# Optimization experiments

Measured on AMD Instinct MI355X. Metric: run time of the kernel, lower is better.

## Reference

```python
import jax, jax.numpy as jnp
import numpy as np

N, R, E, H, D_MAX = 1024, 8192, 1024, 4, 48
DH = E // H
P_EDGE = 16.0 / R  # average in-degree ~16


def setup_inputs() -> dict:
    key = jax.random.key(0)
    ks = jax.random.split(key, 6)
    s = 0.02
    return {
        "target": jax.random.normal(ks[0], (N, E), jnp.float32),
        "source": jax.random.normal(ks[1], (R, E), jnp.float32),
        "adj": (jax.random.uniform(ks[2], (N, R)) < P_EDGE).astype(jnp.float32),
        "W_trans": jax.random.normal(ks[3], (E, E), jnp.float32) * s,
        "b_trans": jnp.zeros((E,), jnp.float32),
        "in_proj_w": jax.random.normal(ks[4], (3 * E, E), jnp.float32) * s,
        "in_proj_b": jnp.zeros((3 * E,), jnp.float32),
        "out_w": jax.random.normal(ks[5], (E, E), jnp.float32) * s,
        "out_b": jnp.zeros((E,), jnp.float32),
        "unit_id": 0,
    }


def reference(target, source, adj, W_trans, b_trans, in_proj_w, in_proj_b, out_w, out_b, unit_id):
    # source = relu(trans_fc(source))
    src = jax.nn.relu(source @ W_trans.T + b_trans)  # [R, E]

    # build padded neighbor index lists (torch loops per node; here vectorized)
    deg = adj.sum(axis=1).astype(jnp.int32)                # [N]
    order = jnp.argsort(-adj, axis=1)[:, :D_MAX]           # stable: 1-columns first, ascending col idx
    valid = jnp.arange(D_MAX)[None, :] < deg[:, None]      # [N, D] True = real neighbor
    neigh = jnp.where(valid, order, 0)                     # pad with index 0 (masked, like torch)
    kv_in = src[neigh]                                     # [N, D, E] gathered neighbor feats

    # nn.MultiheadAttention: q=target (len-1 query), k=v=padded neighbors
    Wq, Wk, Wv = jnp.split(in_proj_w, 3, axis=0)
    bq, bk, bv = jnp.split(in_proj_b, 3)
    q = (target @ Wq.T + bq).reshape(-1, H, DH)            # [N, H, dh]
    k = (kv_in @ Wk.T + bk).reshape(-1, D_MAX, H, DH)      # [N, D, H, dh]
    v = (kv_in @ Wv.T + bv).reshape(-1, D_MAX, H, DH)

    scores = jnp.einsum('nhd,nkhd->nhk', q, k) / np.float32(np.sqrt(DH))  # [N, H, D]
    # key_padding_mask: padded slots -> -inf; give zero-degree nodes one dummy
    # unmasked slot so softmax stays finite (their output is zeroed below)
    safe_valid = valid.at[:, 0].set(valid[:, 0] | (deg == 0))
    scores = jnp.where(safe_valid[:, None, :], scores, -jnp.inf)
    attn = jax.nn.softmax(scores, axis=-1)
    out = jnp.einsum('nhk,nkhd->nhd', attn, v).reshape(-1, E)
    out = out @ out_w.T + out_b

    # scatter back: inactive (degree-0) nodes stay zero, like att_res_padded
    return jnp.where((deg > 0)[:, None], out, jnp.zeros((), out.dtype))
```

## Files before the change

### kernel.cpp

```cpp
#include <hip/hip_runtime.h>

#define N_NODES 1024
#define R_SRC   8192
#define E_DIM   1024
#define H_HEADS 4
#define DH_DIM  256
#define D_MAXN  48

typedef __attribute__((ext_vector_type(8))) short short8;
typedef __attribute__((ext_vector_type(4))) float f32x4;

__device__ __forceinline__ unsigned short f2bf(float f) {
    unsigned u = __float_as_uint(f);
    unsigned r = u + 0x7fffu + ((u >> 16) & 1u);
    return (unsigned short)(r >> 16);
}
__device__ __forceinline__ float bf2f(unsigned short b) {
    return __uint_as_float(((unsigned)b) << 16);
}
__device__ __forceinline__ void gload16(const void* g, void* l) {
    __builtin_amdgcn_global_load_lds(
        (const __attribute__((address_space(1))) unsigned int*)g,
        (__attribute__((address_space(3))) unsigned int*)l,
        16, 0, 0);
}
template<int N> __device__ __forceinline__ void vwait() {
    if constexpr (N == 8)       asm volatile("s_waitcnt vmcnt(8)" ::: "memory");
    else if constexpr (N == 6)  asm volatile("s_waitcnt vmcnt(6)" ::: "memory");
    else if constexpr (N == 1)  asm volatile("s_waitcnt vmcnt(1)" ::: "memory");
    else                        asm volatile("s_waitcnt vmcnt(0)" ::: "memory");
}

struct GD {
    const unsigned short* A;
    const unsigned short* B;
    const float* bias;
    void* C;
    int N, K, nbx, relu, outbf;
    const int* rowmask;
};

template<int BM, int BN>
__global__ __launch_bounds__(512) void gemm_t(GD d0, GD d1, int split)
{
    constexpr int AI = BM / 64;
    constexpr int BI = BN / 64;
    constexpr int VN = AI + BI;
    constexpr int FM = BM / 32;
    constexpr int FN = BN / 64;

    __shared__ __align__(16) unsigned short lds[3][(BM + BN) * 64];

    int bid = blockIdx.x;
    const int nwg = gridDim.x;
    bid = (bid & 7) * (nwg >> 3) + (bid >> 3);

    GD d; int q;
    if (bid < split) { d = d0; q = bid; }
    else             { d = d1; q = bid - split; }
    const int m0 = (q / d.nbx) * BM;
    const int n0 = (q % d.nbx) * BN;
    const int K  = d.K;

    const int t = threadIdx.x;
    const int w = t >> 6, l = t & 63;
    const int wm = w >> 2, wn = w & 3;

    const int trow = t >> 3, tkc = t & 7;
    const int tswz = tkc ^ (trow & 7);
    const unsigned short* gA[AI];
    const unsigned short* gB[BI];
#pragma unroll
    for (int i = 0; i < AI; ++i)
        gA[i] = d.A + (size_t)(m0 + i * 64 + trow) * K + tswz * 8;
#pragma unroll
    for (int i = 0; i < BI; ++i)
        gB[i] = d.B + (size_t)(n0 + i * 64 + trow) * K + tswz * 8;

    f32x4 acc[FM][FN] = {};

    auto STAGE = [&](int c, int kt) {
        const int ko = kt * 64;
#pragma unroll
        for (int i = 0; i < AI; ++i)
            gload16(gA[i] + ko, &lds[c][(i * 512 + t) * 8]);
#pragma unroll
        for (int i = 0; i < BI; ++i)
            gload16(gB[i] + ko, &lds[c][BM * 64 + (i * 512 + t) * 8]);
    };

    const int nt = K / 64;
    STAGE(0, 0);
    STAGE(1, 1);
    vwait<VN>();
    __builtin_amdgcn_s_barrier();

    const int lr = l & 15, hi = l >> 4;
    const int rsw = l & 7;
    const int cs0 = ((0 + hi) ^ rsw) * 8;
    const int cs1 = ((4 + hi) ^ rsw) * 8;
    const int abase = (wm * (BM / 2) + lr) * 64;
    const int bbase = BM * 64 + (wn * 64 + lr) * 64;

    for (int kt = 0; kt < nt; ++kt) {
        const int cur = kt % 3;
        if (kt + 2 < nt) STAGE((kt + 2) % 3, kt + 2);

        const unsigned short* Ls = &lds[cur][0];

        short8 bv[FN][2];
#pragma unroll
        for (int fj = 0; fj < FN; ++fj) {
            bv[fj][0] = *(const short8*)&Ls[bbase + fj * 1024 + cs0];
            bv[fj][1] = *(const short8*)&Ls[bbase + fj * 1024 + cs1];
        }
#pragma unroll
        for (int g = 0; g < FM; g += 4) {
            short8 av[4][2];
#pragma unroll
            for (int fi = 0; fi < 4; ++fi) {
                av[fi][0] = *(const short8*)&Ls[abase + (g + fi) * 1024 + cs0];
                av[fi][1] = *(const short8*)&Ls[abase + (g + fi) * 1024 + cs1];
            }
            __builtin_amdgcn_s_setprio(1);
#pragma unroll
            for (int ks = 0; ks < 2; ++ks)
#pragma unroll
                for (int fi = 0; fi < 4; ++fi)
#pragma unroll
                    for (int fj = 0; fj < FN; ++fj)
                        acc[g + fi][fj] = __builtin_amdgcn_mfma_f32_16x16x32_bf16(
                            av[fi][ks], bv[fj][ks], acc[g + fi][fj], 0, 0, 0);
            __builtin_amdgcn_s_setprio(0);
        }

        asm volatile("" ::: "memory");
        __builtin_amdgcn_s_barrier();
        if (kt + 2 < nt) {
            vwait<VN>();
        } else {
            vwait<0>();
        }
        __builtin_amdgcn_s_barrier();
    }

#pragma unroll
    for (int fj = 0; fj < FN; ++fj) {
        const int c = n0 + wn * 64 + fj * 16 + lr;
        const float bvs = d.bias[c];
#pragma unroll
        for (int fi = 0; fi < FM; ++fi) {
            const int rb = m0 + wm * (BM / 2) + fi * 16 + hi * 4;
#pragma unroll
            for (int qq = 0; qq < 4; ++qq) {
                const int r = rb + qq;
                float x = acc[fi][fj][qq] + bvs;
                if (d.relu) x = fmaxf(x, 0.0f);
                if (d.rowmask && d.rowmask[r] == 0) x = 0.0f;
                if (d.outbf) ((unsigned short*)d.C)[(size_t)r * d.N + c] = f2bf(x);
                else         ((float*)d.C)[(size_t)r * d.N + c] = x;
            }
        }
    }
}

struct GS {
    const unsigned short* A;
    const unsigned short* B;
    const float* bias;
    void* C;
    int lda, ldb, ldc, K, relu, outbf;
    long long azs, bzs, czs;
    int bias_zs;
    const int* rowmask;
};

__global__ __launch_bounds__(256) void gemm_s(GS g)
{
    const int z = blockIdx.z;
    const unsigned short* A = g.A + (size_t)((long long)z * g.azs);
    const unsigned short* B = g.B + (size_t)((long long)z * g.bzs);
    const float* bias = g.bias ? g.bias + (size_t)z * g.bias_zs : nullptr;

    __shared__ __align__(16) unsigned short S[128 * 32];

    const int t = threadIdx.x;
    const int m0 = blockIdx.y * 64;
    const int n0 = blockIdx.x * 64;
    const int w = t >> 6, l = t & 63;
    const int wrow = (w >> 1) * 32;
    const int wcol = (w & 1) * 32;
    const int lr = l & 15;
    const int kg = (l >> 4) * 8;

    f32x4 acc[2][2] = {};

    const unsigned short* gp[2];
    unsigned short* lp[2];
    {
        const int c0 = t;
        gp[0] = A + (size_t)(m0 + (c0 >> 2)) * g.lda + (c0 & 3) * 8;
        lp[0] = &S[c0 * 8];
        const int c1 = t;
        gp[1] = B + (size_t)(n0 + (c1 >> 2)) * g.ldb + (c1 & 3) * 8;
        lp[1] = &S[2048 + c1 * 8];
    }

    for (int k0 = 0; k0 < g.K; k0 += 32) {
        gload16(gp[0] + k0, lp[0]);
        gload16(gp[1] + k0, lp[1]);
        __syncthreads();

        short8 af[2], bw[2];
#pragma unroll
        for (int i = 0; i < 2; ++i)
            af[i] = *(const short8*)&S[(wrow + i * 16 + lr) * 32 + kg];
#pragma unroll
        for (int j = 0; j < 2; ++j)
            bw[j] = *(const short8*)&S[2048 + (wcol + j * 16 + lr) * 32 + kg];
#pragma unroll
        for (int i = 0; i < 2; ++i)
#pragma unroll
            for (int j = 0; j < 2; ++j)
                acc[i][j] = __builtin_amdgcn_mfma_f32_16x16x32_bf16(
                    af[i], bw[j], acc[i][j], 0, 0, 0);
        __syncthreads();
    }

#pragma unroll
    for (int j = 0; j < 2; ++j) {
        const int c = n0 + wcol + j * 16 + lr;
        const float bv = bias ? bias[c] : 0.0f;
#pragma unroll
        for (int i = 0; i < 2; ++i) {
            const int rbase = m0 + wrow + i * 16 + (l >> 4) * 4;
#pragma unroll
            for (int qq = 0; qq < 4; ++qq) {
                const int r = rbase + qq;
                float x = acc[i][j][qq] + bv;
                if (g.relu) x = fmaxf(x, 0.0f);
                if (g.rowmask && g.rowmask[r] == 0) x = 0.0f;
                if (g.outbf)
                    ((unsigned short*)g.C)[(size_t)((long long)z * g.czs) + (size_t)r * g.ldc + c] = f2bf(x);
                else
                    ((float*)g.C)[(size_t)((long long)z * g.czs) + (size_t)r * g.ldc + c] = x;
            }
        }
    }
}

struct ConvArgs {
    const float* s[6];
    unsigned short* d[6];
    unsigned off[7];
};

__global__ __launch_bounds__(256) void pre_kernel(
    const float* __restrict__ adj, int* __restrict__ neigh, int* __restrict__ deg,
    ConvArgs a, const float* __restrict__ inw_f, unsigned short* __restrict__ WkT,
    int nconv)
{
    const int t = threadIdx.x;

    if (blockIdx.x >= (unsigned)(N_NODES + nconv)) {
        __shared__ float tile[64][65];
        const int tb = blockIdx.x - N_NODES - nconv;
        const int h = tb >> 6, rem = tb & 63;
        const int e0 = (rem >> 2) * 64, d0 = (rem & 3) * 64;
        const int r = t >> 2, c4 = (t & 3) * 16;
        const float* tsrc = inw_f + (size_t)(E_DIM + h * 256 + d0 + r) * E_DIM + e0 + c4;
#pragma unroll
        for (int jj = 0; jj < 4; ++jj) {
            float4 v = ((const float4*)tsrc)[jj];
            tile[r][c4 + jj * 4 + 0] = v.x;
            tile[r][c4 + jj * 4 + 1] = v.y;
            tile[r][c4 + jj * 4 + 2] = v.z;
            tile[r][c4 + jj * 4 + 3] = v.w;
        }
        __syncthreads();
        const int er = t >> 2, dc = (t & 3) * 16;
        unsigned short* wout = WkT + ((size_t)h * E_DIM + e0 + er) * 256 + d0 + dc;
#pragma unroll
        for (int jj = 0; jj < 4; ++jj) {
            ushort4 o;
            o.x = f2bf(tile[dc + jj * 4 + 0][er]);
            o.y = f2bf(tile[dc + jj * 4 + 1][er]);
            o.z = f2bf(tile[dc + jj * 4 + 2][er]);
            o.w = f2bf(tile[dc + jj * 4 + 3][er]);
            ((ushort4*)wout)[jj] = o;
        }
        return;
    }

    if (blockIdx.x >= (unsigned)N_NODES) {
        unsigned i = (blockIdx.x - N_NODES) * 256 + t;
        if (i >= a.off[6]) return;
        int seg = 0;
#pragma unroll
        for (int s = 1; s < 6; ++s) seg += (i >= a.off[s]);
        unsigned j = i - a.off[seg];
        float4 v = ((const float4*)a.s[seg])[j];
        ushort4 o;
        o.x = f2bf(v.x); o.y = f2bf(v.y); o.z = f2bf(v.z); o.w = f2bf(v.w);
        ((ushort4*)a.d[seg])[j] = o;
        return;
    }

    const int n    = blockIdx.x;
    const int w    = t >> 6;
    const int lane = t & 63;
    const float* row = adj + (size_t)n * R_SRC;

    __shared__ int s_cnt[4];
    __shared__ int s_idx[4][D_MAXN];

    const int seg0 = w * (R_SRC / 4);
    const unsigned long long lower = (1ULL << lane) - 1ULL;
    int total = 0;

    for (int base = seg0; base < seg0 + R_SRC / 4; base += 256) {
        const float v0 = row[base + lane];
        const float v1 = row[base + 64 + lane];
        const float v2 = row[base + 128 + lane];
        const float v3 = row[base + 192 + lane];
        const unsigned long long m0 = __ballot(v0 != 0.0f);
        const unsigned long long m1 = __ballot(v1 != 0.0f);
        const unsigned long long m2 = __ballot(v2 != 0.0f);
        const unsigned long long m3 = __ballot(v3 != 0.0f);
        int p;
        p = total + __popcll(m0 & lower);
        if (v0 != 0.0f && p < D_MAXN) s_idx[w][p] = base + lane;
        total += __popcll(m0);
        p = total + __popcll(m1 & lower);
        if (v1 != 0.0f && p < D_MAXN) s_idx[w][p] = base + 64 + lane;
        total += __popcll(m1);
        p = total + __popcll(m2 & lower);
        if (v2 != 0.0f && p < D_MAXN) s_idx[w][p] = base + 128 + lane;
        total += __popcll(m2);
        p = total + __popcll(m3 & lower);
        if (v3 != 0.0f && p < D_MAXN) s_idx[w][p] = base + 192 + lane;
        total += __popcll(m3);
    }
    if (lane == 0) s_cnt[w] = total;
    __syncthreads();

    int start = 0;
#pragma unroll
    for (int i = 0; i < 4; ++i) if (i < w) start += s_cnt[i];
    const int degree = s_cnt[0] + s_cnt[1] + s_cnt[2] + s_cnt[3];
    const int nstore = total < D_MAXN ? total : D_MAXN;
    if (lane < nstore) {
        const int gpos = start + lane;
        if (gpos < D_MAXN) neigh[n * D_MAXN + gpos] = s_idx[w][lane];
    }
    if (t == 0) deg[n] = degree;
}

__global__ __launch_bounds__(256) void gather_ctx(
    const float* __restrict__ Ahat, const unsigned short* __restrict__ srcrel,
    const int* __restrict__ neigh, const int* __restrict__ deg,
    unsigned short* __restrict__ ctx)
{
    const int n = blockIdx.x;
    const int t = threadIdx.x;
    const int h = t >> 6;
    const int lane = t & 63;

    unsigned short* crow = ctx + ((size_t)n * H_HEADS + h) * E_DIM + lane * 16;
    const int degree = deg[n];
    if (degree == 0) {
        ushort4 z4 = {0, 0, 0, 0};
#pragma unroll
        for (int j = 0; j < 4; ++j) ((ushort4*)crow)[j] = z4;
        return;
    }
    const int dv = degree < D_MAXN ? degree : D_MAXN;

    __shared__ int s_neigh[D_MAXN];
    if (t < dv) s_neigh[t] = neigh[n * D_MAXN + t];
    __syncthreads();

    float a[16];
    {
        const float4* ap = (const float4*)(Ahat + (size_t)n * (H_HEADS * E_DIM) + h * E_DIM + lane * 16);
#pragma unroll
        for (int j = 0; j < 4; ++j) {
            float4 v = ap[j];
            a[j * 4 + 0] = v.x; a[j * 4 + 1] = v.y; a[j * 4 + 2] = v.z; a[j * 4 + 3] = v.w;
        }
    }

    float m = -3.4e38f, sum = 0.0f;
    float cacc[16];
#pragma unroll
    for (int i = 0; i < 16; ++i) cacc[i] = 0.0f;

    for (int d = 0; d < dv; ++d) {
        const int r = s_neigh[d];
        const ushort4* rp = (const ushort4*)(srcrel + (size_t)r * E_DIM + lane * 16);
        float e[16];
#pragma unroll
        for (int j = 0; j < 4; ++j) {
            ushort4 v = rp[j];
            e[j * 4 + 0] = bf2f(v.x); e[j * 4 + 1] = bf2f(v.y);
            e[j * 4 + 2] = bf2f(v.z); e[j * 4 + 3] = bf2f(v.w);
        }
        float s = 0.0f;
#pragma unroll
        for (int i = 0; i < 16; ++i) s = fmaf(a[i], e[i], s);
#pragma unroll
        for (int off = 32; off > 0; off >>= 1) s += __shfl_xor(s, off);
        s *= 0.0625f;

        if (s > m) {
            const float f = __expf(m - s);
            sum *= f;
#pragma unroll
            for (int i = 0; i < 16; ++i) cacc[i] *= f;
            m = s;
        }
        const float wgt = __expf(s - m);
        sum += wgt;
#pragma unroll
        for (int i = 0; i < 16; ++i) cacc[i] = fmaf(wgt, e[i], cacc[i]);
    }

    const float inv = 1.0f / sum;
#pragma unroll
    for (int j = 0; j < 4; ++j) {
        ushort4 o;
        o.x = f2bf(cacc[j * 4 + 0] * inv);
        o.y = f2bf(cacc[j * 4 + 1] * inv);
        o.z = f2bf(cacc[j * 4 + 2] * inv);
        o.w = f2bf(cacc[j * 4 + 3] * inv);
        ((ushort4*)crow)[j] = o;
    }
}

extern "C" void kernel_launch(void* const* d_in, const int* in_sizes, int n_in,
                              void* d_out, int out_size, void* d_ws, size_t ws_size,
                              hipStream_t stream)
{
    const float* target  = (const float*)d_in[0];
    const float* source  = (const float*)d_in[1];
    const float* adj     = (const float*)d_in[2];
    const float* W_trans = (const float*)d_in[3];
    const float* b_trans = (const float*)d_in[4];
    const float* in_w    = (const float*)d_in[5];
    const float* in_b    = (const float*)d_in[6];
    const float* out_w   = (const float*)d_in[7];
    const float* out_b   = (const float*)d_in[8];
    float* out = (float*)d_out;

    char* ws = (char*)d_ws;
    unsigned short* src_bf    = (unsigned short*)ws; ws += (size_t)R_SRC * E_DIM * 2;
    unsigned short* wt_bf     = (unsigned short*)ws; ws += (size_t)E_DIM * E_DIM * 2;
    unsigned short* inw_bf    = (unsigned short*)ws; ws += (size_t)3 * E_DIM * E_DIM * 2;
    unsigned short* outw_bf   = (unsigned short*)ws; ws += (size_t)E_DIM * E_DIM * 2;
    unsigned short* tgt_bf    = (unsigned short*)ws; ws += (size_t)N_NODES * E_DIM * 2;
    unsigned short* srcrel_bf = (unsigned short*)ws; ws += (size_t)R_SRC * E_DIM * 2;
    unsigned short* WkT_bf    = (unsigned short*)ws; ws += (size_t)H_HEADS * E_DIM * DH_DIM * 2;
    unsigned short* Q_bf      = (unsigned short*)ws; ws += (size_t)N_NODES * E_DIM * 2;
    float*          Ahat      = (float*)ws;         ws += (size_t)N_NODES * H_HEADS * E_DIM * 4;
    unsigned short* ctx_bf    = (unsigned short*)ws; ws += (size_t)N_NODES * H_HEADS * E_DIM * 2;
    unsigned short* attn_bf   = (unsigned short*)ws; ws += (size_t)N_NODES * E_DIM * 2;
    int*            neigh     = (int*)ws;            ws += (size_t)N_NODES * D_MAXN * 4;
    int*            deg       = (int*)ws;            ws += (size_t)N_NODES * 4;

    const size_t EE = (size_t)E_DIM * E_DIM;

    {
        ConvArgs a;
        const unsigned sz4[6] = {
            (unsigned)((size_t)R_SRC * E_DIM / 4),
            (unsigned)(EE / 4),
            (unsigned)(EE / 4),
            (unsigned)(EE / 4),
            (unsigned)(EE / 4),
            (unsigned)((size_t)N_NODES * E_DIM / 4)};
        a.s[0] = source;        a.d[0] = src_bf;
        a.s[1] = W_trans;       a.d[1] = wt_bf;
        a.s[2] = in_w;          a.d[2] = inw_bf;
        a.s[3] = in_w + 2 * EE; a.d[3] = inw_bf + 2 * EE;
        a.s[4] = out_w;         a.d[4] = outw_bf;
        a.s[5] = target;        a.d[5] = tgt_bf;
        a.off[0] = 0;
        for (int i = 0; i < 6; ++i) a.off[i + 1] = a.off[i] + sz4[i];
        const int nconv = (int)((a.off[6] + 255) / 256);
        pre_kernel<<<N_NODES + nconv + 256, 256, 0, stream>>>(
            adj, neigh, deg, a, in_w, WkT_bf, nconv);
    }

    {
        GD ds;
        ds.A = src_bf; ds.B = wt_bf; ds.bias = b_trans; ds.C = srcrel_bf;
        ds.N = E_DIM; ds.K = E_DIM; ds.nbx = E_DIM / 256; ds.relu = 1; ds.outbf = 1;
        ds.rowmask = nullptr;
        const int sblocks = (R_SRC / 128) * (E_DIM / 256);
        gemm_t<128, 256><<<sblocks, 512, 0, stream>>>(ds, ds, sblocks);
    }

    {
        GS g;
        g.A = tgt_bf; g.B = inw_bf; g.bias = in_b; g.C = Q_bf;
        g.lda = E_DIM; g.ldb = E_DIM; g.ldc = E_DIM; g.K = E_DIM;
        g.relu = 0; g.outbf = 1; g.azs = 0; g.bzs = 0; g.czs = 0; g.bias_zs = 0;
        g.rowmask = nullptr;
        gemm_s<<<dim3(E_DIM / 64, N_NODES / 64, 1), 256, 0, stream>>>(g);
    }

    {
        GS g;
        g.A = Q_bf; g.B = WkT_bf; g.bias = nullptr; g.C = Ahat;
        g.lda = E_DIM; g.ldb = DH_DIM; g.ldc = H_HEADS * E_DIM; g.K = DH_DIM;
        g.relu = 0; g.outbf = 0;
        g.azs = DH_DIM;
        g.bzs = (long long)E_DIM * DH_DIM;
        g.czs = E_DIM;
        g.bias_zs = 0; g.rowmask = nullptr;
        gemm_s<<<dim3(E_DIM / 64, N_NODES / 64, H_HEADS), 256, 0, stream>>>(g);
    }

    gather_ctx<<<N_NODES, 256, 0, stream>>>(Ahat, srcrel_bf, neigh, deg, ctx_bf);

    {
        GS g;
        g.A = ctx_bf; g.B = inw_bf + 2 * EE; g.bias = in_b + 2 * E_DIM; g.C = attn_bf;
        g.lda = H_HEADS * E_DIM; g.ldb = E_DIM; g.ldc = E_DIM; g.K = E_DIM;
        g.relu = 0; g.outbf = 1;
        g.azs = E_DIM;
        g.bzs = (long long)DH_DIM * E_DIM;
        g.czs = DH_DIM;
        g.bias_zs = DH_DIM; g.rowmask = nullptr;
        gemm_s<<<dim3(DH_DIM / 64, N_NODES / 64, H_HEADS), 256, 0, stream>>>(g);
    }

    {
        GS g;
        g.A = attn_bf; g.B = outw_bf; g.bias = out_b; g.C = out;
        g.lda = E_DIM; g.ldb = E_DIM; g.ldc = E_DIM; g.K = E_DIM;
        g.relu = 0; g.outbf = 0; g.azs = 0; g.bzs = 0; g.czs = 0; g.bias_zs = 0;
        g.rowmask = deg;
        gemm_s<<<dim3(E_DIM / 64, N_NODES / 64, 1), 256, 0, stream>>>(g);
    }
}
```

Measured before the change: 126.5 us.

## Fuse Q projection into pre-kernel and unroll neighbor gather by two

Moves the Q = target·Wq^T + bq projection into the pre-processing kernel as 256 extra blocks. These blocks read fp32 target and weights, convert them to bf16 in registers and run MFMA directly, so the separate bf16 conversion of target and Wq and one GEMM launch go away. The gather/online-softmax loop is also unrolled to handle two neighbors per iteration, so their loads and reductions can overlap. In exchange, the fused Q GEMM uses a simple unpipelined LDS tile with two barriers per K step and no double buffering, and it runs alongside the adjacency and conversion work.

```diff
diff --git a/kernel.cpp b/kernel.cpp
--- a/kernel.cpp
+++ b/kernel.cpp
@@ -250,17 +250,84 @@
 }
 
 struct ConvArgs {
-    const float* s[6];
-    unsigned short* d[6];
-    unsigned off[7];
+    const float* s[4];
+    unsigned short* d[4];
+    unsigned off[5];
 };
 
 __global__ __launch_bounds__(256) void pre_kernel(
     const float* __restrict__ adj, int* __restrict__ neigh, int* __restrict__ deg,
-    ConvArgs a, const float* __restrict__ inw_f, unsigned short* __restrict__ WkT,
-    int nconv)
+    ConvArgs a, const float* __restrict__ inw_f, const float* __restrict__ tgt_f,
+    const float* __restrict__ in_b, unsigned short* __restrict__ WkT,
+    unsigned short* __restrict__ Q_bf, int nconv)
 {
     const int t = threadIdx.x;
+
+    if (blockIdx.x >= (unsigned)(N_NODES + nconv + 256)) {
+        __shared__ __align__(16) unsigned short QS[2][64 * 32];
+        const int qb = blockIdx.x - (N_NODES + nconv + 256);
+        const int m0 = (qb >> 4) * 64;
+        const int n0 = (qb & 15) * 64;
+        const int w = t >> 6, l = t & 63;
+        const int wrow = (w >> 1) * 32;
+        const int wcol = (w & 1) * 32;
+        const int lr = l & 15;
+        const int kg = (l >> 4) * 8;
+        const int row = t >> 2, k8 = (t & 3) * 8;
+
+        const float* ga = tgt_f + (size_t)(m0 + row) * E_DIM + k8;
+        const float* gb = inw_f + (size_t)(n0 + row) * E_DIM + k8;
+
+        f32x4 acc[2][2] = {};
+
+        for (int k0 = 0; k0 < E_DIM; k0 += 32) {
+            float4 a0 = *(const float4*)(ga + k0);
+            float4 a1 = *(const float4*)(ga + k0 + 4);
+            float4 b0 = *(const float4*)(gb + k0);
+            float4 b1 = *(const float4*)(gb + k0 + 4);
+            short8 av, bv;
+            av[0] = (short)f2bf(a0.x); av[1] = (short)f2bf(a0.y);
+            av[2] = (short)f2bf(a0.z); av[3] = (short)f2bf(a0.w);
+            av[4] = (short)f2bf(a1.x); av[5] = (short)f2bf(a1.y);
+            av[6] = (short)f2bf(a1.z); av[7] = (short)f2bf(a1.w);
+            bv[0] = (short)f2bf(b0.x); bv[1] = (short)f2bf(b0.y);
+            bv[2] = (short)f2bf(b0.z); bv[3] = (short)f2bf(b0.w);
+            bv[4] = (short)f2bf(b1.x); bv[5] = (short)f2bf(b1.y);
+            bv[6] = (short)f2bf(b1.z); bv[7] = (short)f2bf(b1.w);
+            *(short8*)&QS[0][row * 32 + k8] = av;
+            *(short8*)&QS[1][row * 32 + k8] = bv;
+            __syncthreads();
+
+            short8 af[2], bw[2];
+#pragma unroll
+            for (int i = 0; i < 2; ++i)
+                af[i] = *(const short8*)&QS[0][(wrow + i * 16 + lr) * 32 + kg];
+#pragma unroll
+            for (int j = 0; j < 2; ++j)
+                bw[j] = *(const short8*)&QS[1][(wcol + j * 16 + lr) * 32 + kg];
+#pragma unroll
+            for (int i = 0; i < 2; ++i)
+#pragma unroll
+                for (int j = 0; j < 2; ++j)
+                    acc[i][j] = __builtin_amdgcn_mfma_f32_16x16x32_bf16(
+                        af[i], bw[j], acc[i][j], 0, 0, 0);
+            __syncthreads();
+        }
+
+#pragma unroll
+        for (int j = 0; j < 2; ++j) {
+            const int c = n0 + wcol + j * 16 + lr;
+            const float bv = in_b[c];
+#pragma unroll
+            for (int i = 0; i < 2; ++i) {
+                const int rbase = m0 + wrow + i * 16 + (l >> 4) * 4;
+#pragma unroll
+                for (int qq = 0; qq < 4; ++qq)
+                    Q_bf[(size_t)(rbase + qq) * E_DIM + c] = f2bf(acc[i][j][qq] + bv);
+            }
+        }
+        return;
+    }
 
     if (blockIdx.x >= (unsigned)(N_NODES + nconv)) {
         __shared__ float tile[64][65];
@@ -294,10 +361,10 @@
 
     if (blockIdx.x >= (unsigned)N_NODES) {
         unsigned i = (blockIdx.x - N_NODES) * 256 + t;
-        if (i >= a.off[6]) return;
+        if (i >= a.off[4]) return;
         int seg = 0;
 #pragma unroll
-        for (int s = 1; s < 6; ++s) seg += (i >= a.off[s]);
+        for (int s = 1; s < 4; ++s) seg += (i >= a.off[s]);
         unsigned j = i - a.off[seg];
         float4 v = ((const float4*)a.s[seg])[j];
         ushort4 o;
@@ -395,9 +462,63 @@
 #pragma unroll
     for (int i = 0; i < 16; ++i) cacc[i] = 0.0f;
 
-    for (int d = 0; d < dv; ++d) {
-        const int r = s_neigh[d];
-        const ushort4* rp = (const ushort4*)(srcrel + (size_t)r * E_DIM + lane * 16);
+    const float scale = 0.0625f;
+
+    int d = 0;
+    for (; d + 1 < dv; d += 2) {
+        const ushort4* rp0 = (const ushort4*)(srcrel + (size_t)s_neigh[d]     * E_DIM + lane * 16);
+        const ushort4* rp1 = (const ushort4*)(srcrel + (size_t)s_neigh[d + 1] * E_DIM + lane * 16);
+        ushort4 w00 = rp0[0], w01 = rp0[1], w02 = rp0[2], w03 = rp0[3];
+        ushort4 w10 = rp1[0], w11 = rp1[1], w12 = rp1[2], w13 = rp1[3];
+        float e0[16], e1[16];
+        e0[0]=bf2f(w00.x); e0[1]=bf2f(w00.y); e0[2]=bf2f(w00.z); e0[3]=bf2f(w00.w);
+        e0[4]=bf2f(w01.x); e0[5]=bf2f(w01.y); e0[6]=bf2f(w01.z); e0[7]=bf2f(w01.w);
+        e0[8]=bf2f(w02.x); e0[9]=bf2f(w02.y); e0[10]=bf2f(w02.z); e0[11]=bf2f(w02.w);
+        e0[12]=bf2f(w03.x); e0[13]=bf2f(w03.y); e0[14]=bf2f(w03.z); e0[15]=bf2f(w03.w);
+        e1[0]=bf2f(w10.x); e1[1]=bf2f(w10.y); e1[2]=bf2f(w10.z); e1[3]=bf2f(w10.w);
+        e1[4]=bf2f(w11.x); e1[5]=bf2f(w11.y); e1[6]=bf2f(w11.z); e1[7]=bf2f(w11.w);
+        e1[8]=bf2f(w12.x); e1[9]=bf2f(w12.y); e1[10]=bf2f(w12.z); e1[11]=bf2f(w12.w);
+        e1[12]=bf2f(w13.x); e1[13]=bf2f(w13.y); e1[14]=bf2f(w13.z); e1[15]=bf2f(w13.w);
+
+        float s0 = 0.0f, s1 = 0.0f;
+#pragma unroll
+        for (int i = 0; i < 16; ++i) { s0 = fmaf(a[i], e0[i], s0); s1 = fmaf(a[i], e1[i], s1); }
+#pragma unroll
+        for (int off = 32; off > 0; off >>= 1) {
+            s0 += __shfl_xor(s0, off);
+            s1 += __shfl_xor(s1, off);
+        }
+        s0 *= scale; s1 *= scale;
+
+        if (s0 > m) {
+            const float f = __expf(m - s0);
+            sum *= f;
+#pragma unroll
+            for (int i = 0; i < 16; ++i) cacc[i] *= f;
+            m = s0;
+        }
+        {
+            const float wgt = __expf(s0 - m);
+            sum += wgt;
+#pragma unroll
+            for (int i = 0; i < 16; ++i) cacc[i] = fmaf(wgt, e0[i], cacc[i]);
+        }
+        if (s1 > m) {
+            const float f = __expf(m - s1);
+            sum *= f;
+#pragma unroll
+            for (int i = 0; i < 16; ++i) cacc[i] *= f;
+            m = s1;
+        }
+        {
+            const float wgt = __expf(s1 - m);
+            sum += wgt;
+#pragma unroll
+            for (int i = 0; i < 16; ++i) cacc[i] = fmaf(wgt, e1[i], cacc[i]);
+        }
+    }
+    for (; d < dv; ++d) {
+        const ushort4* rp = (const ushort4*)(srcrel + (size_t)s_neigh[d] * E_DIM + lane * 16);
         float e[16];
 #pragma unroll
         for (int j = 0; j < 4; ++j) {
@@ -410,8 +531,7 @@
         for (int i = 0; i < 16; ++i) s = fmaf(a[i], e[i], s);
 #pragma unroll
         for (int off = 32; off > 0; off >>= 1) s += __shfl_xor(s, off);
-        s *= 0.0625f;
-
+        s *= scale;
         if (s > m) {
             const float f = __expf(m - s);
             sum *= f;
@@ -455,9 +575,8 @@
     char* ws = (char*)d_ws;
     unsigned short* src_bf    = (unsigned short*)ws; ws += (size_t)R_SRC * E_DIM * 2;
     unsigned short* wt_bf     = (unsigned short*)ws; ws += (size_t)E_DIM * E_DIM * 2;
-    unsigned short* inw_bf    = (unsigned short*)ws; ws += (size_t)3 * E_DIM * E_DIM * 2;
+    unsigned short* wv_bf     = (unsigned short*)ws; ws += (size_t)E_DIM * E_DIM * 2;
     unsigned short* outw_bf   = (unsigned short*)ws; ws += (size_t)E_DIM * E_DIM * 2;
-    unsigned short* tgt_bf    = (unsigned short*)ws; ws += (size_t)N_NODES * E_DIM * 2;
     unsigned short* srcrel_bf = (unsigned short*)ws; ws += (size_t)R_SRC * E_DIM * 2;
     unsigned short* WkT_bf    = (unsigned short*)ws; ws += (size_t)H_HEADS * E_DIM * DH_DIM * 2;
     unsigned short* Q_bf      = (unsigned short*)ws; ws += (size_t)N_NODES * E_DIM * 2;
@@ -471,24 +590,20 @@
 
     {
         ConvArgs a;
-        const unsigned sz4[6] = {
+        const unsigned sz4[4] = {
             (unsigned)((size_t)R_SRC * E_DIM / 4),
             (unsigned)(EE / 4),
             (unsigned)(EE / 4),
-            (unsigned)(EE / 4),
-            (unsigned)(EE / 4),
-            (unsigned)((size_t)N_NODES * E_DIM / 4)};
+            (unsigned)(EE / 4)};
         a.s[0] = source;        a.d[0] = src_bf;
         a.s[1] = W_trans;       a.d[1] = wt_bf;
-        a.s[2] = in_w;          a.d[2] = inw_bf;
-        a.s[3] = in_w + 2 * EE; a.d[3] = inw_bf + 2 * EE;
-        a.s[4] = out_w;         a.d[4] = outw_bf;
-        a.s[5] = target;        a.d[5] = tgt_bf;
+        a.s[2] = in_w + 2 * EE; a.d[2] = wv_bf;
+        a.s[3] = out_w;         a.d[3] = outw_bf;
         a.off[0] = 0;
-        for (int i = 0; i < 6; ++i) a.off[i + 1] = a.off[i] + sz4[i];
-        const int nconv = (int)((a.off[6] + 255) / 256);
-        pre_kernel<<<N_NODES + nconv + 256, 256, 0, stream>>>(
-            adj, neigh, deg, a, in_w, WkT_bf, nconv);
+        for (int i = 0; i < 4; ++i) a.off[i + 1] = a.off[i] + sz4[i];
+        const int nconv = (int)((a.off[4] + 255) / 256);
+        pre_kernel<<<N_NODES + nconv + 256 + 256, 256, 0, stream>>>(
+            adj, neigh, deg, a, in_w, target, in_b, WkT_bf, Q_bf, nconv);
     }
 
     {
@@ -498,15 +613,6 @@
         ds.rowmask = nullptr;
         const int sblocks = (R_SRC / 128) * (E_DIM / 256);
         gemm_t<128, 256><<<sblocks, 512, 0, stream>>>(ds, ds, sblocks);
-    }
-
-    {
-        GS g;
-        g.A = tgt_bf; g.B = inw_bf; g.bias = in_b; g.C = Q_bf;
-        g.lda = E_DIM; g.ldb = E_DIM; g.ldc = E_DIM; g.K = E_DIM;
-        g.relu = 0; g.outbf = 1; g.azs = 0; g.bzs = 0; g.czs = 0; g.bias_zs = 0;
-        g.rowmask = nullptr;
-        gemm_s<<<dim3(E_DIM / 64, N_NODES / 64, 1), 256, 0, stream>>>(g);
     }
 
     {
@@ -525,7 +631,7 @@
 
     {
         GS g;
-        g.A = ctx_bf; g.B = inw_bf + 2 * EE; g.bias = in_b + 2 * E_DIM; g.C = attn_bf;
+        g.A = ctx_bf; g.B = wv_bf; g.bias = in_b + 2 * E_DIM; g.C = attn_bf;
         g.lda = H_HEADS * E_DIM; g.ldb = E_DIM; g.ldc = E_DIM; g.K = E_DIM;
         g.relu = 0; g.outbf = 1;
         g.azs = E_DIM;
```

Measured after the change: 124.0 us. About the same (-2.0%).
